# Optimization experiments

Hardware: AMD Instinct MI355X
Metric: run time of the kernel (lower is better)

The kernel has to match this reference:

```python
import jax, jax.numpy as jnp
import numpy as np

N_NODES = 50000
N_EDGES = 800000
IN_DIM = 256
OUT_DIM = 256


def setup_inputs() -> dict:
    key = jax.random.key(0)
    k1, k2, k3, k4 = jax.random.split(key, 4)
    feature = jax.random.normal(k1, (N_NODES, IN_DIM), dtype=jnp.float32)
    weight = jax.random.normal(k2, (IN_DIM, OUT_DIM), dtype=jnp.float32)
    src = jax.random.randint(k3, (N_EDGES,), 0, N_NODES, dtype=jnp.int32)
    dst = jax.random.randint(k4, (N_EDGES,), 0, N_NODES, dtype=jnp.int32)
    return {"feature": feature, "weight": weight, "src": src, "dst": dst}


def reference(feature, weight, src, dst):
    # Kernel math: for each edge (s -> d): out[d] += feature[s] @ W.
    # By linearity this equals segment_sum(feature[src] by dst) @ W,
    # which avoids materializing the [E, OUT_DIM] transformed edge features.
    agg = jax.ops.segment_sum(feature[src], dst, num_segments=N_NODES)  # [N, in_dim]
    out = agg @ weight  # [N, out_dim]
    return out
```

## Files before the change

kernel.cpp:

```cpp
#include <hip/hip_runtime.h>
#include <hip/hip_bf16.h>

#define IN_DIM 256
#define OUT_DIM 256
#define CAP 64

typedef __attribute__((ext_vector_type(8))) short bf16x8;
typedef __attribute__((ext_vector_type(4))) float f32x4;

__device__ inline unsigned short bfbits(float x) {
    __hip_bfloat16 h = __float2bfloat16(x);
    return *(unsigned short*)&h;
}
__device__ inline float4 bf4_to_f4(ushort4 u) {
    float4 r;
    r.x = __uint_as_float((unsigned)u.x << 16);
    r.y = __uint_as_float((unsigned)u.y << 16);
    r.z = __uint_as_float((unsigned)u.z << 16);
    r.w = __uint_as_float((unsigned)u.w << 16);
    return r;
}


__global__ void prep_kernel(const float* __restrict__ feat, const float* __restrict__ W,
                            unsigned short* __restrict__ featb, unsigned short* __restrict__ Wt,
                            int* __restrict__ cursor, int nfeat, int FB, int ncur) {
    int b = blockIdx.x, tid = threadIdx.x;
    if (b < FB) {
        int i = (b * 256 + tid) * 4;
        if (i < nfeat) {
            float4 v = *(const float4*)(feat + i);
            ushort4 u;
            u.x = bfbits(v.x); u.y = bfbits(v.y); u.z = bfbits(v.z); u.w = bfbits(v.w);
            *(ushort4*)(featb + i) = u;
        }
    } else if (b < FB + OUT_DIM) {
        int n = b - FB;
        Wt[n * IN_DIM + tid] = bfbits(W[tid * OUT_DIM + n]);
    } else {
        int i = ((b - FB - OUT_DIM) * 256 + tid) * 4;
        if (i < ncur) *(int4*)(cursor + i) = make_int4(0, 0, 0, 0);
    }
}


__global__ void bucket_kernel(const int* __restrict__ src, const int* __restrict__ dst,
                              int* __restrict__ cursor, unsigned short* __restrict__ bucket, int E) {
    int e = blockIdx.x * 256 + threadIdx.x;
    if (e < E) {
        int d = dst[e];
        int pos = atomicAdd(&cursor[d << 4], 1);
        if (pos < CAP) bucket[d * CAP + pos] = (unsigned short)src[e];
    }
}


__global__ __launch_bounds__(256) void aggregate_bf16(const unsigned short* __restrict__ featb,
                                                      const unsigned short* __restrict__ bucket,
                                                      const int* __restrict__ cursor,
                                                      unsigned short* __restrict__ agg, int N) {
    int node = blockIdx.x * 4 + (threadIdx.x >> 6);
    int lane = threadIdx.x & 63;
    if (node >= N) return;
    int cnt = min(cursor[node << 4], CAP);
    const unsigned short* bp = bucket + node * CAP;
    float4 a0 = make_float4(0.f, 0.f, 0.f, 0.f), a1 = a0, a2 = a0, a3 = a0;
    int e = 0;
    for (; e + 4 <= cnt; e += 4) {
        int s0 = bp[e], s1 = bp[e + 1], s2 = bp[e + 2], s3 = bp[e + 3];
        float4 v0 = bf4_to_f4(((const ushort4*)(featb + (size_t)s0 * IN_DIM))[lane]);
        float4 v1 = bf4_to_f4(((const ushort4*)(featb + (size_t)s1 * IN_DIM))[lane]);
        float4 v2 = bf4_to_f4(((const ushort4*)(featb + (size_t)s2 * IN_DIM))[lane]);
        float4 v3 = bf4_to_f4(((const ushort4*)(featb + (size_t)s3 * IN_DIM))[lane]);
        a0.x += v0.x; a0.y += v0.y; a0.z += v0.z; a0.w += v0.w;
        a1.x += v1.x; a1.y += v1.y; a1.z += v1.z; a1.w += v1.w;
        a2.x += v2.x; a2.y += v2.y; a2.z += v2.z; a2.w += v2.w;
        a3.x += v3.x; a3.y += v3.y; a3.z += v3.z; a3.w += v3.w;
    }
    for (; e < cnt; ++e) {
        float4 v = bf4_to_f4(((const ushort4*)(featb + (size_t)bp[e] * IN_DIM))[lane]);
        a0.x += v.x; a0.y += v.y; a0.z += v.z; a0.w += v.w;
    }
    a0.x += a1.x + a2.x + a3.x;
    a0.y += a1.y + a2.y + a3.y;
    a0.z += a1.z + a2.z + a3.z;
    a0.w += a1.w + a2.w + a3.w;
    ushort4 o;
    o.x = bfbits(a0.x); o.y = bfbits(a0.y); o.z = bfbits(a0.z); o.w = bfbits(a0.w);
    ((ushort4*)(agg + (size_t)node * IN_DIM))[lane] = o;
}


__global__ __launch_bounds__(256) void gemm_mfma(const unsigned short* __restrict__ A,
                                                 const unsigned short* __restrict__ Bt,
                                                 float* __restrict__ C, int M) {
    __shared__ unsigned short sA[64][40];
    __shared__ unsigned short sB[128][40];
    int tid = threadIdx.x;
    int wave = tid >> 6, lane = tid & 63;
    int m16 = lane & 15, quad = lane >> 4;
    int rb = blockIdx.y * 64, cb = blockIdx.x * 128;
    f32x4 acc[8] = {};

    for (int k0 = 0; k0 < IN_DIM; k0 += 32) {
        {
            int r = tid >> 2, g = tid & 3;
            int gr = rb + r;
            ulonglong2 v; v.x = 0; v.y = 0;
            if (gr < M) v = *(const ulonglong2*)(A + (size_t)gr * IN_DIM + k0 + g * 8);
            *(ulonglong2*)&sA[r][g * 8] = v;
        }
        #pragma unroll
        for (int t = 0; t < 2; ++t) {
            int f = tid + t * 256;
            int nrow = f >> 2, g = f & 3;
            *(ulonglong2*)&sB[nrow][g * 8] =
                *(const ulonglong2*)(Bt + (size_t)(cb + nrow) * IN_DIM + k0 + g * 8);
        }
        __syncthreads();
        bf16x8 afrag = *(const bf16x8*)&sA[wave * 16 + m16][quad * 8];
        #pragma unroll
        for (int nt = 0; nt < 8; ++nt) {
            bf16x8 bfrag = *(const bf16x8*)&sB[nt * 16 + m16][quad * 8];
            acc[nt] = __builtin_amdgcn_mfma_f32_16x16x32_bf16(afrag, bfrag, acc[nt], 0, 0, 0);
        }
        __syncthreads();
    }
    #pragma unroll
    for (int nt = 0; nt < 8; ++nt) {
        #pragma unroll
        for (int r = 0; r < 4; ++r) {
            int gr = rb + wave * 16 + quad * 4 + r;
            if (gr < M) C[(size_t)gr * OUT_DIM + cb + nt * 16 + m16] = acc[nt][r];
        }
    }
}


extern "C" void kernel_launch(void* const* d_in, const int* in_sizes, int n_in,
                              void* d_out, int out_size, void* d_ws, size_t ws_size,
                              hipStream_t stream) {
    const float* feature = (const float*)d_in[0];
    const float* weight  = (const float*)d_in[1];
    const int*   src     = (const int*)d_in[2];
    const int*   dst     = (const int*)d_in[3];
    float*       out     = (float*)d_out;

    int N = in_sizes[0] / IN_DIM;
    int E = in_sizes[2];
    int nfeat = N * IN_DIM;
    int ncur = N * 16;

    char* ws = (char*)d_ws;
    unsigned short* featb  = (unsigned short*)ws;
    unsigned short* agg    = featb + (size_t)nfeat;
    unsigned short* Wt     = agg + (size_t)nfeat;
    int*            cursor = (int*)((char*)(Wt + IN_DIM * OUT_DIM));
    unsigned short* bucket = (unsigned short*)(cursor + ncur);

    int FB = (nfeat / 4 + 255) / 256;
    int CB = (ncur / 4 + 255) / 256;
    prep_kernel<<<FB + OUT_DIM + CB, 256, 0, stream>>>(feature, weight, featb, Wt, cursor,
                                                       nfeat, FB, ncur);
    bucket_kernel<<<(E + 255) / 256, 256, 0, stream>>>(src, dst, cursor, bucket, E);
    aggregate_bf16<<<(N + 3) / 4, 256, 0, stream>>>(featb, bucket, cursor, agg, N);

    dim3 ggrid(OUT_DIM / 128, (N + 63) / 64);
    gemm_mfma<<<ggrid, 256, 0, stream>>>(agg, Wt, out, N);
}
```

Before: 218.8 us.

## Fuse aggregation into GEMM and merge bucketing with bf16 prep

Aggregation and the MFMA GEMM now run in one kernel: each wave gathers 16 nodes into shared memory and multiplies them by the full 256-column bf16 weight, which it reads directly from global memory. This removes the round trip of the bf16 agg buffer through HBM and one kernel launch. Bucketing is merged into the prep kernel, and cursor zeroing moves to a hipMemsetAsync. The risks are lower occupancy from 16 accumulators per wave, uncached Wt reads in every block, and far fewer blocks for the gather (N/64 instead of N/4), which limits latency hiding.

Result: slower. 417.4 us (+90.8%).

```diff
diff --git a/kernel.cpp b/kernel.cpp
--- a/kernel.cpp
+++ b/kernel.cpp
@@ -22,116 +22,94 @@
 }
 
 
-__global__ void prep_kernel(const float* __restrict__ feat, const float* __restrict__ W,
-                            unsigned short* __restrict__ featb, unsigned short* __restrict__ Wt,
-                            int* __restrict__ cursor, int nfeat, int FB, int ncur) {
+__global__ __launch_bounds__(256) void prep_bucket(
+        const float* __restrict__ feat, const float* __restrict__ W,
+        const int* __restrict__ src, const int* __restrict__ dst,
+        unsigned short* __restrict__ featb, unsigned short* __restrict__ Wt,
+        int* __restrict__ cursor, unsigned short* __restrict__ bucket,
+        int E, int BKT, int FB, int nfeat) {
     int b = blockIdx.x, tid = threadIdx.x;
-    if (b < FB) {
-        int i = (b * 256 + tid) * 4;
+    if (b < BKT) {
+        int e = b * 256 + tid;
+        if (e < E) {
+            int d = dst[e];
+            int pos = atomicAdd(&cursor[d << 4], 1);
+            if (pos < CAP) bucket[d * CAP + pos] = (unsigned short)src[e];
+        }
+    } else if (b < BKT + FB) {
+        int i = ((b - BKT) * 256 + tid) * 4;
         if (i < nfeat) {
             float4 v = *(const float4*)(feat + i);
             ushort4 u;
             u.x = bfbits(v.x); u.y = bfbits(v.y); u.z = bfbits(v.z); u.w = bfbits(v.w);
             *(ushort4*)(featb + i) = u;
         }
-    } else if (b < FB + OUT_DIM) {
-        int n = b - FB;
+    } else {
+        int n = b - BKT - FB;
         Wt[n * IN_DIM + tid] = bfbits(W[tid * OUT_DIM + n]);
-    } else {
-        int i = ((b - FB - OUT_DIM) * 256 + tid) * 4;
-        if (i < ncur) *(int4*)(cursor + i) = make_int4(0, 0, 0, 0);
     }
 }
 
 
-__global__ void bucket_kernel(const int* __restrict__ src, const int* __restrict__ dst,
-                              int* __restrict__ cursor, unsigned short* __restrict__ bucket, int E) {
-    int e = blockIdx.x * 256 + threadIdx.x;
-    if (e < E) {
-        int d = dst[e];
-        int pos = atomicAdd(&cursor[d << 4], 1);
-        if (pos < CAP) bucket[d * CAP + pos] = (unsigned short)src[e];
-    }
-}
-
-
-__global__ __launch_bounds__(256) void aggregate_bf16(const unsigned short* __restrict__ featb,
-                                                      const unsigned short* __restrict__ bucket,
-                                                      const int* __restrict__ cursor,
-                                                      unsigned short* __restrict__ agg, int N) {
-    int node = blockIdx.x * 4 + (threadIdx.x >> 6);
-    int lane = threadIdx.x & 63;
-    if (node >= N) return;
-    int cnt = min(cursor[node << 4], CAP);
-    const unsigned short* bp = bucket + node * CAP;
-    float4 a0 = make_float4(0.f, 0.f, 0.f, 0.f), a1 = a0, a2 = a0, a3 = a0;
-    int e = 0;
-    for (; e + 4 <= cnt; e += 4) {
-        int s0 = bp[e], s1 = bp[e + 1], s2 = bp[e + 2], s3 = bp[e + 3];
-        float4 v0 = bf4_to_f4(((const ushort4*)(featb + (size_t)s0 * IN_DIM))[lane]);
-        float4 v1 = bf4_to_f4(((const ushort4*)(featb + (size_t)s1 * IN_DIM))[lane]);
-        float4 v2 = bf4_to_f4(((const ushort4*)(featb + (size_t)s2 * IN_DIM))[lane]);
-        float4 v3 = bf4_to_f4(((const ushort4*)(featb + (size_t)s3 * IN_DIM))[lane]);
-        a0.x += v0.x; a0.y += v0.y; a0.z += v0.z; a0.w += v0.w;
-        a1.x += v1.x; a1.y += v1.y; a1.z += v1.z; a1.w += v1.w;
-        a2.x += v2.x; a2.y += v2.y; a2.z += v2.z; a2.w += v2.w;
-        a3.x += v3.x; a3.y += v3.y; a3.z += v3.z; a3.w += v3.w;
-    }
-    for (; e < cnt; ++e) {
-        float4 v = bf4_to_f4(((const ushort4*)(featb + (size_t)bp[e] * IN_DIM))[lane]);
-        a0.x += v.x; a0.y += v.y; a0.z += v.z; a0.w += v.w;
-    }
-    a0.x += a1.x + a2.x + a3.x;
-    a0.y += a1.y + a2.y + a3.y;
-    a0.z += a1.z + a2.z + a3.z;
-    a0.w += a1.w + a2.w + a3.w;
-    ushort4 o;
-    o.x = bfbits(a0.x); o.y = bfbits(a0.y); o.z = bfbits(a0.z); o.w = bfbits(a0.w);
-    ((ushort4*)(agg + (size_t)node * IN_DIM))[lane] = o;
-}
-
-
-__global__ __launch_bounds__(256) void gemm_mfma(const unsigned short* __restrict__ A,
-                                                 const unsigned short* __restrict__ Bt,
-                                                 float* __restrict__ C, int M) {
-    __shared__ unsigned short sA[64][40];
-    __shared__ unsigned short sB[128][40];
+__global__ __launch_bounds__(256, 4) void agg_gemm(
+        const unsigned short* __restrict__ featb,
+        const unsigned short* __restrict__ bucket,
+        const int* __restrict__ cursor,
+        const unsigned short* __restrict__ Wt,
+        float* __restrict__ C, int N) {
+    __shared__ unsigned short sA[4][16][264];
     int tid = threadIdx.x;
     int wave = tid >> 6, lane = tid & 63;
     int m16 = lane & 15, quad = lane >> 4;
-    int rb = blockIdx.y * 64, cb = blockIdx.x * 128;
-    f32x4 acc[8] = {};
+    int rb = blockIdx.x * 64 + wave * 16;
 
+    for (int i = 0; i < 16; ++i) {
+        int node = rb + i;
+        float4 a0 = make_float4(0.f, 0.f, 0.f, 0.f), a1 = a0, a2 = a0, a3 = a0;
+        if (node < N) {
+            int cnt = min(cursor[node << 4], CAP);
+            const unsigned short* bp = bucket + node * CAP;
+            int e = 0;
+            for (; e + 4 <= cnt; e += 4) {
+                int s0 = bp[e], s1 = bp[e + 1], s2 = bp[e + 2], s3 = bp[e + 3];
+                float4 v0 = bf4_to_f4(((const ushort4*)(featb + (size_t)s0 * IN_DIM))[lane]);
+                float4 v1 = bf4_to_f4(((const ushort4*)(featb + (size_t)s1 * IN_DIM))[lane]);
+                float4 v2 = bf4_to_f4(((const ushort4*)(featb + (size_t)s2 * IN_DIM))[lane]);
+                float4 v3 = bf4_to_f4(((const ushort4*)(featb + (size_t)s3 * IN_DIM))[lane]);
+                a0.x += v0.x; a0.y += v0.y; a0.z += v0.z; a0.w += v0.w;
+                a1.x += v1.x; a1.y += v1.y; a1.z += v1.z; a1.w += v1.w;
+                a2.x += v2.x; a2.y += v2.y; a2.z += v2.z; a2.w += v2.w;
+                a3.x += v3.x; a3.y += v3.y; a3.z += v3.z; a3.w += v3.w;
+            }
+            for (; e < cnt; ++e) {
+                float4 v = bf4_to_f4(((const ushort4*)(featb + (size_t)bp[e] * IN_DIM))[lane]);
+                a0.x += v.x; a0.y += v.y; a0.z += v.z; a0.w += v.w;
+            }
+            a0.x += a1.x + a2.x + a3.x;
+            a0.y += a1.y + a2.y + a3.y;
+            a0.z += a1.z + a2.z + a3.z;
+            a0.w += a1.w + a2.w + a3.w;
+        }
+        ushort4 o;
+        o.x = bfbits(a0.x); o.y = bfbits(a0.y); o.z = bfbits(a0.z); o.w = bfbits(a0.w);
+        *(ushort4*)&sA[wave][i][lane * 4] = o;
+    }
+
+    f32x4 acc[16] = {};
     for (int k0 = 0; k0 < IN_DIM; k0 += 32) {
-        {
-            int r = tid >> 2, g = tid & 3;
-            int gr = rb + r;
-            ulonglong2 v; v.x = 0; v.y = 0;
-            if (gr < M) v = *(const ulonglong2*)(A + (size_t)gr * IN_DIM + k0 + g * 8);
-            *(ulonglong2*)&sA[r][g * 8] = v;
-        }
-        #pragma unroll
-        for (int t = 0; t < 2; ++t) {
-            int f = tid + t * 256;
-            int nrow = f >> 2, g = f & 3;
-            *(ulonglong2*)&sB[nrow][g * 8] =
-                *(const ulonglong2*)(Bt + (size_t)(cb + nrow) * IN_DIM + k0 + g * 8);
-        }
-        __syncthreads();
-        bf16x8 afrag = *(const bf16x8*)&sA[wave * 16 + m16][quad * 8];
-        #pragma unroll
-        for (int nt = 0; nt < 8; ++nt) {
-            bf16x8 bfrag = *(const bf16x8*)&sB[nt * 16 + m16][quad * 8];
+        bf16x8 afrag = *(const bf16x8*)&sA[wave][m16][k0 + quad * 8];
+        #pragma unroll 4
+        for (int nt = 0; nt < 16; ++nt) {
+            bf16x8 bfrag = *(const bf16x8*)(Wt + (size_t)(nt * 16 + m16) * IN_DIM + k0 + quad * 8);
             acc[nt] = __builtin_amdgcn_mfma_f32_16x16x32_bf16(afrag, bfrag, acc[nt], 0, 0, 0);
         }
-        __syncthreads();
     }
     #pragma unroll
-    for (int nt = 0; nt < 8; ++nt) {
+    for (int nt = 0; nt < 16; ++nt) {
         #pragma unroll
         for (int r = 0; r < 4; ++r) {
-            int gr = rb + wave * 16 + quad * 4 + r;
-            if (gr < M) C[(size_t)gr * OUT_DIM + cb + nt * 16 + m16] = acc[nt][r];
+            int gr = rb + quad * 4 + r;
+            if (gr < N) C[(size_t)gr * OUT_DIM + nt * 16 + m16] = acc[nt][r];
         }
     }
 }
@@ -153,18 +131,16 @@
 
     char* ws = (char*)d_ws;
     unsigned short* featb  = (unsigned short*)ws;
-    unsigned short* agg    = featb + (size_t)nfeat;
-    unsigned short* Wt     = agg + (size_t)nfeat;
-    int*            cursor = (int*)((char*)(Wt + IN_DIM * OUT_DIM));
+    unsigned short* Wt     = featb + (size_t)nfeat;
+    int*            cursor = (int*)(Wt + IN_DIM * OUT_DIM);
     unsigned short* bucket = (unsigned short*)(cursor + ncur);
 
-    int FB = (nfeat / 4 + 255) / 256;
-    int CB = (ncur / 4 + 255) / 256;
-    prep_kernel<<<FB + OUT_DIM + CB, 256, 0, stream>>>(feature, weight, featb, Wt, cursor,
-                                                       nfeat, FB, ncur);
-    bucket_kernel<<<(E + 255) / 256, 256, 0, stream>>>(src, dst, cursor, bucket, E);
-    aggregate_bf16<<<(N + 3) / 4, 256, 0, stream>>>(featb, bucket, cursor, agg, N);
+    int FB  = (nfeat / 4 + 255) / 256;
+    int BKT = (E + 255) / 256;
 
-    dim3 ggrid(OUT_DIM / 128, (N + 63) / 64);
-    gemm_mfma<<<ggrid, 256, 0, stream>>>(agg, Wt, out, N);
+    hipMemsetAsync(cursor, 0, (size_t)ncur * sizeof(int), stream);
+    prep_bucket<<<BKT + FB + OUT_DIM, 256, 0, stream>>>(feature, weight, src, dst,
+                                                        featb, Wt, cursor, bucket,
+                                                        E, BKT, FB, nfeat);
+    agg_gemm<<<(N + 63) / 64, 256, 0, stream>>>(featb, bucket, cursor, Wt, out, N);
 }
```

## Slice bf16 features into 32-column planes so gathers hit cache-resident slices

Applied to the files above, without the earlier changes.

Stores the bf16 feature and aggregate matrices as eight column slices of 32 columns, each a contiguous N x 32 plane. The aggregation kernel now assigns each block one slice and a chunk of 64 nodes, so the gathered data per slice (about 3.2 MB) can stay in L2/LLC instead of random 512-byte row gathers over the full 25 MB matrix. The GEMM reads A from the sliced layout, and cursor zeroing moves from the prep kernel to hipMemsetAsync. In exchange, each gather is only 64 bytes per edge, bucket indices are re-read once per slice, and each wave needs a cross-lane shuffle reduction per node.

New measurement: 345.0 us. 1.58x slower.

```diff
diff --git a/kernel.cpp b/kernel.cpp
--- a/kernel.cpp
+++ b/kernel.cpp
@@ -4,6 +4,8 @@
 #define IN_DIM 256
 #define OUT_DIM 256
 #define CAP 64
+#define NSLICE 8
+#define SCOLS 32
 
 typedef __attribute__((ext_vector_type(8))) short bf16x8;
 typedef __attribute__((ext_vector_type(4))) float f32x4;
@@ -12,19 +14,12 @@
     __hip_bfloat16 h = __float2bfloat16(x);
     return *(unsigned short*)&h;
 }
-__device__ inline float4 bf4_to_f4(ushort4 u) {
-    float4 r;
-    r.x = __uint_as_float((unsigned)u.x << 16);
-    r.y = __uint_as_float((unsigned)u.y << 16);
-    r.z = __uint_as_float((unsigned)u.z << 16);
-    r.w = __uint_as_float((unsigned)u.w << 16);
-    return r;
-}
 
 
-__global__ void prep_kernel(const float* __restrict__ feat, const float* __restrict__ W,
-                            unsigned short* __restrict__ featb, unsigned short* __restrict__ Wt,
-                            int* __restrict__ cursor, int nfeat, int FB, int ncur) {
+__global__ __launch_bounds__(256) void prep_kernel(
+        const float* __restrict__ feat, const float* __restrict__ W,
+        unsigned short* __restrict__ featb, unsigned short* __restrict__ Wt,
+        int N, int nfeat, int FB) {
     int b = blockIdx.x, tid = threadIdx.x;
     if (b < FB) {
         int i = (b * 256 + tid) * 4;
@@ -32,20 +27,20 @@
             float4 v = *(const float4*)(feat + i);
             ushort4 u;
             u.x = bfbits(v.x); u.y = bfbits(v.y); u.z = bfbits(v.z); u.w = bfbits(v.w);
-            *(ushort4*)(featb + i) = u;
+            int node = i >> 8, c = i & 255;
+            *(ushort4*)(featb + (size_t)(c >> 5) * N * SCOLS
+                              + (size_t)node * SCOLS + (c & 31)) = u;
         }
-    } else if (b < FB + OUT_DIM) {
+    } else {
         int n = b - FB;
         Wt[n * IN_DIM + tid] = bfbits(W[tid * OUT_DIM + n]);
-    } else {
-        int i = ((b - FB - OUT_DIM) * 256 + tid) * 4;
-        if (i < ncur) *(int4*)(cursor + i) = make_int4(0, 0, 0, 0);
     }
 }
 
 
-__global__ void bucket_kernel(const int* __restrict__ src, const int* __restrict__ dst,
-                              int* __restrict__ cursor, unsigned short* __restrict__ bucket, int E) {
+__global__ __launch_bounds__(256) void bucket_kernel(
+        const int* __restrict__ src, const int* __restrict__ dst,
+        int* __restrict__ cursor, unsigned short* __restrict__ bucket, int E) {
     int e = blockIdx.x * 256 + threadIdx.x;
     if (e < E) {
         int d = dst[e];
@@ -55,39 +50,51 @@
 }
 
 
-__global__ __launch_bounds__(256) void aggregate_bf16(const unsigned short* __restrict__ featb,
-                                                      const unsigned short* __restrict__ bucket,
-                                                      const int* __restrict__ cursor,
-                                                      unsigned short* __restrict__ agg, int N) {
-    int node = blockIdx.x * 4 + (threadIdx.x >> 6);
-    int lane = threadIdx.x & 63;
-    if (node >= N) return;
-    int cnt = min(cursor[node << 4], CAP);
-    const unsigned short* bp = bucket + node * CAP;
-    float4 a0 = make_float4(0.f, 0.f, 0.f, 0.f), a1 = a0, a2 = a0, a3 = a0;
-    int e = 0;
-    for (; e + 4 <= cnt; e += 4) {
-        int s0 = bp[e], s1 = bp[e + 1], s2 = bp[e + 2], s3 = bp[e + 3];
-        float4 v0 = bf4_to_f4(((const ushort4*)(featb + (size_t)s0 * IN_DIM))[lane]);
-        float4 v1 = bf4_to_f4(((const ushort4*)(featb + (size_t)s1 * IN_DIM))[lane]);
-        float4 v2 = bf4_to_f4(((const ushort4*)(featb + (size_t)s2 * IN_DIM))[lane]);
-        float4 v3 = bf4_to_f4(((const ushort4*)(featb + (size_t)s3 * IN_DIM))[lane]);
-        a0.x += v0.x; a0.y += v0.y; a0.z += v0.z; a0.w += v0.w;
-        a1.x += v1.x; a1.y += v1.y; a1.z += v1.z; a1.w += v1.w;
-        a2.x += v2.x; a2.y += v2.y; a2.z += v2.z; a2.w += v2.w;
-        a3.x += v3.x; a3.y += v3.y; a3.z += v3.z; a3.w += v3.w;
+__global__ __launch_bounds__(256) void agg_slice(
+        const unsigned short* __restrict__ featb,
+        const unsigned short* __restrict__ bucket,
+        const int* __restrict__ cursor,
+        unsigned short* __restrict__ agg, int N) {
+    int slice = blockIdx.x & (NSLICE - 1);
+    int chunk = blockIdx.x >> 3;
+    int tid = threadIdx.x;
+    int wave = tid >> 6, lane = tid & 63;
+    int e4 = lane >> 4, c2 = lane & 15;
+    const unsigned short* fs = featb + (size_t)slice * N * SCOLS;
+    unsigned short*       as = agg   + (size_t)slice * N * SCOLS;
+    int base = chunk * 64 + wave * 16;
+
+    for (int i = 0; i < 16; ++i) {
+        int node = base + i;
+        if (node >= N) break;
+        int cnt = min(__builtin_nontemporal_load(&cursor[node << 4]), CAP);
+        const unsigned short* bp = bucket + (size_t)node * CAP;
+        float ax = 0.f, ay = 0.f;
+        int e = 0;
+        for (; e + 8 <= cnt; e += 8) {
+            int s0 = bp[e + e4], s1 = bp[e + 4 + e4];
+            unsigned u0 = *(const unsigned*)(fs + (size_t)s0 * SCOLS + c2 * 2);
+            unsigned u1 = *(const unsigned*)(fs + (size_t)s1 * SCOLS + c2 * 2);
+            ax += __uint_as_float(u0 << 16);
+            ay += __uint_as_float(u0 & 0xffff0000u);
+            ax += __uint_as_float(u1 << 16);
+            ay += __uint_as_float(u1 & 0xffff0000u);
+        }
+        for (; e < cnt; e += 4) {
+            if (e + e4 < cnt) {
+                int s0 = bp[e + e4];
+                unsigned u0 = *(const unsigned*)(fs + (size_t)s0 * SCOLS + c2 * 2);
+                ax += __uint_as_float(u0 << 16);
+                ay += __uint_as_float(u0 & 0xffff0000u);
+            }
+        }
+        ax += __shfl_xor(ax, 16); ay += __shfl_xor(ay, 16);
+        ax += __shfl_xor(ax, 32); ay += __shfl_xor(ay, 32);
+        if (lane < 16) {
+            unsigned o = (unsigned)bfbits(ax) | ((unsigned)bfbits(ay) << 16);
+            *(unsigned*)(as + (size_t)node * SCOLS + c2 * 2) = o;
+        }
     }
-    for (; e < cnt; ++e) {
-        float4 v = bf4_to_f4(((const ushort4*)(featb + (size_t)bp[e] * IN_DIM))[lane]);
-        a0.x += v.x; a0.y += v.y; a0.z += v.z; a0.w += v.w;
-    }
-    a0.x += a1.x + a2.x + a3.x;
-    a0.y += a1.y + a2.y + a3.y;
-    a0.z += a1.z + a2.z + a3.z;
-    a0.w += a1.w + a2.w + a3.w;
-    ushort4 o;
-    o.x = bfbits(a0.x); o.y = bfbits(a0.y); o.z = bfbits(a0.z); o.w = bfbits(a0.w);
-    ((ushort4*)(agg + (size_t)node * IN_DIM))[lane] = o;
 }
 
 
@@ -103,11 +110,12 @@
     f32x4 acc[8] = {};
 
     for (int k0 = 0; k0 < IN_DIM; k0 += 32) {
+        size_t sbase = (size_t)(k0 >> 5) * M * SCOLS;
         {
             int r = tid >> 2, g = tid & 3;
             int gr = rb + r;
             ulonglong2 v; v.x = 0; v.y = 0;
-            if (gr < M) v = *(const ulonglong2*)(A + (size_t)gr * IN_DIM + k0 + g * 8);
+            if (gr < M) v = *(const ulonglong2*)(A + sbase + (size_t)gr * SCOLS + g * 8);
             *(ulonglong2*)&sA[r][g * 8] = v;
         }
         #pragma unroll
@@ -155,15 +163,16 @@
     unsigned short* featb  = (unsigned short*)ws;
     unsigned short* agg    = featb + (size_t)nfeat;
     unsigned short* Wt     = agg + (size_t)nfeat;
-    int*            cursor = (int*)((char*)(Wt + IN_DIM * OUT_DIM));
+    int*            cursor = (int*)(Wt + IN_DIM * OUT_DIM);
     unsigned short* bucket = (unsigned short*)(cursor + ncur);
 
     int FB = (nfeat / 4 + 255) / 256;
-    int CB = (ncur / 4 + 255) / 256;
-    prep_kernel<<<FB + OUT_DIM + CB, 256, 0, stream>>>(feature, weight, featb, Wt, cursor,
-                                                       nfeat, FB, ncur);
+    int NCHUNK = (N + 63) / 64;
+
+    hipMemsetAsync(cursor, 0, (size_t)ncur * sizeof(int), stream);
+    prep_kernel<<<FB + OUT_DIM, 256, 0, stream>>>(feature, weight, featb, Wt, N, nfeat, FB);
     bucket_kernel<<<(E + 255) / 256, 256, 0, stream>>>(src, dst, cursor, bucket, E);
-    aggregate_bf16<<<(N + 3) / 4, 256, 0, stream>>>(featb, bucket, cursor, agg, N);
+    agg_slice<<<NSLICE * NCHUNK, 256, 0, stream>>>(featb, bucket, cursor, agg, N);
 
     dim3 ggrid(OUT_DIM / 128, (N + 63) / 64);
     gemm_mfma<<<ggrid, 256, 0, stream>>>(agg, Wt, out, N);
```
